# Kernel tuning notes

Measured on AMD Instinct MI355X. Metric: run time of the kernel, lower is better.

## Reference

```python
import jax, jax.numpy as jnp
import numpy as np

N = 50000      # nodes
E = 800000     # edges per metapath
M = 3          # metapaths
H = 2          # heads
IN = 128       # in_dim
HID = 64       # hidden
HEAD = HID // H
OUT = 16       # classes
ATT = 128      # atten_dim


def setup_inputs() -> dict:
    key = jax.random.key(0)
    ks = jax.random.split(key, 12)
    s = 0.05
    return {
        "x": jax.random.normal(ks[0], (N, IN), jnp.float32),
        "edge_index": jax.random.randint(ks[1], (M, 2, E), 0, N, dtype=jnp.int64),
        # per-(metapath, head) GCN params
        "W_enc": jax.random.normal(ks[2], (M, H, IN, HID), jnp.float32) * s,
        "b_enc": jnp.zeros((M, H, HID), jnp.float32),
        "W_conv": jax.random.normal(ks[3], (M, H, HID, HID), jnp.float32) * s,
        "b_conv": jnp.zeros((M, H, HID), jnp.float32),
        "W_dec": jax.random.normal(ks[4], (M, H, HID, HEAD), jnp.float32) * s,
        "b_dec": jnp.zeros((M, H, HEAD), jnp.float32),
        # semantic attention params
        "W_s": jax.random.normal(ks[5], (HID, ATT), jnp.float32) * s,
        "b_s": jnp.zeros((ATT,), jnp.float32),
        "q": jax.random.normal(ks[6], (ATT,), jnp.float32) * s,
        # output projection
        "W_o": jax.random.normal(ks[7], (HID, OUT), jnp.float32) * s,
        "b_o": jnp.zeros((OUT,), jnp.float32),
    }


def _lrelu(v, slope=0.1):
    return jnp.where(v > 0, v, slope * v)


def reference(x, edge_index, W_enc, b_enc, W_conv, b_conv, W_dec, b_dec, W_s, b_s, q, W_o, b_o):
    # encoder for all (metapath, head) at once: [M,H,N,HID]
    h = _lrelu(jnp.einsum('ni,mhio->mhno', x, W_enc) + b_enc[:, :, None, :])

    z_list = []
    for m in range(M):  # small fixed number of metapaths
        src = edge_index[m, 0]
        dst = edge_index[m, 1]
        # GCNConv with self-loops + symmetric normalization (PyG semantics)
        deg = jax.ops.segment_sum(jnp.ones(E, jnp.float32), dst, num_segments=N) + 1.0
        inv_sqrt = jax.lax.rsqrt(deg)
        coef = inv_sqrt[src] * inv_sqrt[dst]                 # [E]
        xw = jnp.einsum('hnd,hdo->hno', h[m], W_conv[m])     # [H,N,HID]
        msg = xw[:, src, :] * coef[None, :, None]            # [H,E,HID] gather
        agg = jax.vmap(lambda mm: jax.ops.segment_sum(mm, dst, num_segments=N))(msg)
        agg = agg + xw * (1.0 / deg)[None, :, None]          # self-loop term (norm = 1/deg)
        agg = agg + b_conv[m][:, None, :]
        hh = _lrelu(agg)
        dec = jnp.einsum('hnd,hdo->hno', hh, W_dec[m]) + b_dec[m][:, None, :]  # [H,N,HEAD]
        z_list.append(jnp.transpose(dec, (1, 0, 2)).reshape(N, HID))           # head concat

    zs = jnp.stack(z_list)                                   # [M,N,HID]
    # semantic attention over metapaths
    hs = jnp.tanh(jnp.einsum('mnd,da->mna', zs, W_s) + b_s)
    beta = jax.nn.softmax(jnp.einsum('mna,a->mn', hs, q).mean(axis=1))  # [M]
    Z = jnp.einsum('m,mnd->nd', beta, zs)                    # [N,HID]
    out = jax.nn.log_softmax(Z @ W_o + b_o, axis=-1)         # [N,OUT]
    return out, beta
```

## Files before the change

### kernel.cpp

```cpp
#include <hip/hip_runtime.h>

#define NN 50000
#define EE 800000
#define MM 3
#define HH 2
#define IND 128
#define HIDD 64
#define HEADD 32
#define OUTD 16
#define ATTD 128

#define NBKT 64
#define BSZ 782

#define NG4 200000
#define BBLK 196
#define QCAP 13200

#define GLS 136

typedef unsigned char u8;
typedef unsigned short u16;
typedef unsigned long long u64;
typedef short bf16x8 __attribute__((ext_vector_type(8)));
typedef unsigned short u16x8 __attribute__((ext_vector_type(8)));
typedef u64 u64x2 __attribute__((ext_vector_type(2)));
typedef float f32x2 __attribute__((ext_vector_type(2)));
typedef float f32x4 __attribute__((ext_vector_type(4)));

__device__ __forceinline__ float lrelu(float v) { return v > 0.f ? v : 0.1f * v; }

__device__ __forceinline__ float fast_tanh(float x) {
    float ax = fabsf(x);
    float e = __expf(-2.0f * ax);
    float t = (1.0f - e) * __builtin_amdgcn_rcpf(1.0f + e);
    return copysignf(t, x);
}

__device__ __forceinline__ u16 f2b(float f) {
    union { float f; unsigned int u; } v; v.f = f;
    unsigned int r = v.u + 0x7fffu + ((v.u >> 16) & 1u);
    return (u16)(r >> 16);
}
__device__ __forceinline__ float b2f(u16 u) {
    union { unsigned int u; float f; } v; v.u = ((unsigned int)u) << 16; return v.f;
}

__device__ __forceinline__ u8 f2e4hw(float f) {
    int r = __builtin_amdgcn_cvt_pk_fp8_f32(f, f, 0, false);
    return (u8)(r & 0xff);
}

__global__ __launch_bounds__(256) void k_bucket(const int* __restrict__ ei,
                                                u64* __restrict__ queues,
                                                int* __restrict__ gcur) {
    __shared__ int cnt[NBKT];
    __shared__ int base[NBKT];
    const int m = blockIdx.y, tid = threadIdx.x;
    const int4* s4 = (const int4*)(ei + (size_t)m * 2 * EE);
    const int4* d4 = (const int4*)(ei + (size_t)m * 2 * EE + EE);
    const int q0 = blockIdx.x * 1024;
    if (tid < NBKT) cnt[tid] = 0;
    __syncthreads();
#pragma unroll
    for (int i = 0; i < 4; i++) {
        int q = q0 + i * 256 + tid;
        if (q < NG4) {
            int4 v = d4[q];
            atomicAdd(&cnt[v.x / BSZ], 1);
            atomicAdd(&cnt[v.y / BSZ], 1);
            atomicAdd(&cnt[v.z / BSZ], 1);
            atomicAdd(&cnt[v.w / BSZ], 1);
        }
    }
    __syncthreads();
    if (tid < NBKT) { base[tid] = atomicAdd(&gcur[m * NBKT + tid], cnt[tid]); cnt[tid] = 0; }
    __syncthreads();
#pragma unroll
    for (int i = 0; i < 4; i++) {
        int q = q0 + i * 256 + tid;
        if (q < NG4) {
            int4 dv = d4[q];
            int4 sv = s4[q];
            int ds[4] = {dv.x, dv.y, dv.z, dv.w};
            int ss[4] = {sv.x, sv.y, sv.z, sv.w};
#pragma unroll
            for (int e = 0; e < 4; e++) {
                int b = ds[e] / BSZ;
                int slot = base[b] + atomicAdd(&cnt[b], 1);
                if (slot < QCAP) {
                    u64 pk = ((u64)(unsigned)ds[e] << 32) | (unsigned)ss[e];
                    queues[((size_t)(m * NBKT + b)) * QCAP + slot] = pk;
                }
            }
        }
    }
}

__global__ void k_pscan(const int* __restrict__ gcur, int* __restrict__ pbase) {
    int t = threadIdx.x;
    if (t < MM) {
        int run = 0;
        for (int b = 0; b < NBKT; b++) {
            int L = gcur[t * NBKT + b]; if (L > QCAP) L = QCAP;
            pbase[t * NBKT + b] = run; run += L;
        }
    }
}

__global__ __launch_bounds__(512) void k_csr(const u64* __restrict__ queues,
                                             const int* __restrict__ gcur,
                                             const int* __restrict__ pbase,
                                             int* __restrict__ ofs,
                                             float* __restrict__ rs,
                                             int* __restrict__ sorted) {
    __shared__ int cnt[BSZ];
    __shared__ int wscan[8];
    const int m = blockIdx.y;
    const int b = blockIdx.x;
    const int tid = threadIdx.x;
    const int lane = tid & 63, w = tid >> 6;
    int qlen = gcur[m * NBKT + b]; if (qlen > QCAP) qlen = QCAP;
    const u64* q = queues + ((size_t)(m * NBKT + b)) * QCAP;
    const u64x2* q2 = (const u64x2*)q;
    const int dlo = b * BSZ;
    const int nd = min(dlo + BSZ, NN) - dlo;
    const int n2 = qlen >> 1;
    for (int i = tid; i < BSZ; i += 512) cnt[i] = 0;
    __syncthreads();
    for (int i = tid; i < n2; i += 512) {
        u64x2 e = q2[i];
        atomicAdd(&cnt[(int)(e.x >> 32) - dlo], 1);
        atomicAdd(&cnt[(int)(e.y >> 32) - dlo], 1);
    }
    if (tid == 0 && (qlen & 1))
        atomicAdd(&cnt[(int)(q[qlen - 1] >> 32) - dlo], 1);
    __syncthreads();
    const int c0 = tid * 2;
    int v0 = (c0 < BSZ) ? cnt[c0] : 0;
    int v1 = (c0 + 1 < BSZ) ? cnt[c0 + 1] : 0;
    int s = v0 + v1;
    int vv = s;
    for (int off = 1; off < 64; off <<= 1) { int t = __shfl_up(vv, off); if (lane >= off) vv += t; }
    if (lane == 63) wscan[w] = vv;
    __syncthreads();
    if (tid == 0) { int run = 0; for (int j = 0; j < 8; j++) { int t = wscan[j]; wscan[j] = run; run += t; } }
    __syncthreads();
    int excl = wscan[w] + vv - s;
    int g0 = pbase[m * NBKT + b] + excl;
    int g1 = g0 + v0;
    if (c0 < nd) {
        ofs[(size_t)m * (NN + 1) + dlo + c0] = g0;
        rs[(size_t)m * NN + dlo + c0] = rsqrtf((float)(v0 + 1));
    }
    if (c0 + 1 < nd) {
        ofs[(size_t)m * (NN + 1) + dlo + c0 + 1] = g1;
        rs[(size_t)m * NN + dlo + c0 + 1] = rsqrtf((float)(v1 + 1));
    }
    if (b == NBKT - 1 && tid == 0)
        ofs[(size_t)m * (NN + 1) + NN] = EE;
    __syncthreads();
    if (c0 < BSZ) cnt[c0] = g0;
    if (c0 + 1 < BSZ) cnt[c0 + 1] = g1;
    __syncthreads();
    int* srt = sorted + (size_t)m * EE;
    for (int i = tid; i < n2; i += 512) {
        u64x2 e = q2[i];
        int p0 = atomicAdd(&cnt[(int)(e.x >> 32) - dlo], 1);
        srt[p0] = (int)(e.x & 0xffffffffu);
        int p1 = atomicAdd(&cnt[(int)(e.y >> 32) - dlo], 1);
        srt[p1] = (int)(e.y & 0xffffffffu);
    }
    if (tid == 0 && (qlen & 1)) {
        u64 e = q[qlen - 1];
        int p0 = atomicAdd(&cnt[(int)(e >> 32) - dlo], 1);
        srt[p0] = (int)(e & 0xffffffffu);
    }
}

__global__ __launch_bounds__(256) void k_prep(const float* __restrict__ We, const float* __restrict__ Wc,
                                              const float* __restrict__ Wd, const float* __restrict__ Ws,
                                              u16* __restrict__ wbe, u16* __restrict__ wbc,
                                              u16* __restrict__ wbd, u16* __restrict__ wbs) {
    int t = blockIdx.x * 256 + threadIdx.x;
    if (t >= 11776) return;
    bf16x8 val;
    u16* dst;
    if (t < 6144) {
        int m = t >> 11, r = t & 2047;
        int nt = r >> 8, ks = (r >> 6) & 3, lane = r & 63;
        int n = nt * 16 + (lane & 15), h = n >> 6, o = n & 63;
        int kb = ks * 32 + (lane >> 4) * 8;
        const float* w = We + ((size_t)(m * 2 + h) * 128) * 64;
#pragma unroll
        for (int j = 0; j < 8; j++) val[j] = (short)f2b(w[(size_t)(kb + j) * 64 + o]);
        dst = wbe + ((size_t)m * 2048 + r) * 8;
    } else if (t < 9216) {
        int u = t - 6144;
        int m = u >> 10, r = u & 1023;
        int nt = r >> 7, ks = (r >> 6) & 1, lane = r & 63;
        int h = nt >> 2, o = (nt & 3) * 16 + (lane & 15);
        int kb = ks * 32 + (lane >> 4) * 8;
        const float* w = Wc + ((size_t)(m * 2 + h) * 64) * 64;
#pragma unroll
        for (int j = 0; j < 8; j++) val[j] = (short)f2b(w[(size_t)(kb + j) * 64 + o]);
        dst = wbc + ((size_t)m * 1024 + r) * 8;
    } else if (t < 10752) {
        int u = t - 9216;
        int m = u >> 9, r = u & 511;
        int nt = r >> 7, ks = (r >> 6) & 1, lane = r & 63;
        int h = nt >> 1, o = (nt & 1) * 16 + (lane & 15);
        int kb = ks * 32 + (lane >> 4) * 8;
        const float* w = Wd + ((size_t)(m * 2 + h) * 64) * 32;
#pragma unroll
        for (int j = 0; j < 8; j++) val[j] = (short)f2b(w[(size_t)(kb + j) * 32 + o]);
        dst = wbd + ((size_t)m * 512 + r) * 8;
    } else {
        int r = t - 10752;
        int nt = r >> 7, ks = (r >> 6) & 1, lane = r & 63;
        int n = nt * 16 + (lane & 15);
        int kb = ks * 32 + (lane >> 4) * 8;
#pragma unroll
        for (int j = 0; j < 8; j++) val[j] = (short)f2b(Ws[(size_t)(kb + j) * 128 + n]);
        dst = wbs + (size_t)r * 8;
    }
    *(bf16x8*)dst = val;
}

#define HLS 133
__global__ __launch_bounds__(256) void k_encconv(const float* __restrict__ x,
                                                 const u16* __restrict__ wbe_all,
                                                 const float* __restrict__ be_all,
                                                 const u16* __restrict__ wbc_all,
                                                 const float* __restrict__ rs_all,
                                                 u8* __restrict__ xw_all) {
    __shared__ float hl[64 * HLS];
    const int m = blockIdx.y;
    const int tid = threadIdx.x, lane = tid & 63, wave = tid >> 6;
    const int quad = lane >> 4, c16 = lane & 15;
    const int row = blockIdx.x * 64 + wave * 16 + c16;
    const bool ok = row < NN;
    const bf16x8* wbE = (const bf16x8*)(wbe_all + (size_t)m * 2048 * 8);
    const float* be = be_all + m * 2 * 64;
    const float* rs = rs_all + (size_t)m * NN;
    u8* xw = xw_all + (size_t)m * NN * 128;
    f32x4 zero = {0.f, 0.f, 0.f, 0.f};
    f32x4 acc[8];
#pragma unroll
    for (int nt = 0; nt < 8; nt++) acc[nt] = zero;
#pragma unroll
    for (int ks = 0; ks < 4; ks++) {
        bf16x8 a = {0, 0, 0, 0, 0, 0, 0, 0};
        if (ok) {
            const float* xp = x + (size_t)row * 128 + ks * 32 + quad * 8;
            float4 xa = *(const float4*)xp;
            float4 xb = *(const float4*)(xp + 4);
            a[0] = (short)f2b(xa.x); a[1] = (short)f2b(xa.y);
            a[2] = (short)f2b(xa.z); a[3] = (short)f2b(xa.w);
            a[4] = (short)f2b(xb.x); a[5] = (short)f2b(xb.y);
            a[6] = (short)f2b(xb.z); a[7] = (short)f2b(xb.w);
        }
#pragma unroll
        for (int nt = 0; nt < 8; nt++)
            acc[nt] = __builtin_amdgcn_mfma_f32_16x16x32_bf16(a, wbE[(nt * 4 + ks) * 64 + lane], acc[nt], 0, 0, 0);
    }
    const int rbl = wave * 16 + quad * 4;
#pragma unroll
    for (int nt = 0; nt < 8; nt++) {
        int col = nt * 16 + c16, hh = col >> 6, o = col & 63;
        float bias = be[hh * 64 + o];
#pragma unroll
        for (int j = 0; j < 4; j++) {
            int rl = rbl + j;
            int rg = blockIdx.x * 64 + rl;
            hl[rl * HLS + col] = (rg < NN) ? lrelu(acc[nt][j] + bias) : 0.f;
        }
    }
    __syncthreads();
    const bf16x8* wbC = (const bf16x8*)(wbc_all + (size_t)m * 1024 * 8);
    f32x4 cacc[8];
#pragma unroll
    for (int nt = 0; nt < 8; nt++) cacc[nt] = zero;
    const int rl = wave * 16 + c16;
#pragma unroll
    for (int ks = 0; ks < 2; ks++) {
        bf16x8 a0, a1;
        const float* hp = &hl[rl * HLS + ks * 32 + quad * 8];
#pragma unroll
        for (int j = 0; j < 8; j++) { a0[j] = (short)f2b(hp[j]); a1[j] = (short)f2b(hp[64 + j]); }
#pragma unroll
        for (int nt = 0; nt < 8; nt++)
            cacc[nt] = __builtin_amdgcn_mfma_f32_16x16x32_bf16(nt < 4 ? a0 : a1, wbC[(nt * 2 + ks) * 64 + lane], cacc[nt], 0, 0, 0);
    }
    float rsv[4];
#pragma unroll
    for (int j = 0; j < 4; j++) {
        int r = blockIdx.x * 64 + rbl + j;
        rsv[j] = (r < NN) ? rs[r] * 64.f : 0.f;
    }
#pragma unroll
    for (int nt = 0; nt < 8; nt++) {
        int col = nt * 16 + c16;
#pragma unroll
        for (int j = 0; j < 4; j++) {
            int r = blockIdx.x * 64 + rbl + j;
            if (r < NN) xw[(size_t)r * 128 + col] = f2e4hw(cacc[nt][j] * rsv[j]);
        }
    }
}

__device__ __forceinline__ void acc_fp8x8(f32x2* acc, u64 w) {
    unsigned lo = (unsigned)w, hi = (unsigned)(w >> 32);
    acc[0] += __builtin_amdgcn_cvt_pk_f32_fp8(lo, false);
    acc[1] += __builtin_amdgcn_cvt_pk_f32_fp8(lo, true);
    acc[2] += __builtin_amdgcn_cvt_pk_f32_fp8(hi, false);
    acc[3] += __builtin_amdgcn_cvt_pk_f32_fp8(hi, true);
}

__global__ __launch_bounds__(512) void k_gpost(const int* __restrict__ sorted_all,
                                               const int* __restrict__ ofs_all,
                                               const float* __restrict__ rs_all,
                                               const u8* __restrict__ xw_all,
                                               const float* __restrict__ bconv_all,
                                               const u16* __restrict__ wbd_all,
                                               const float* __restrict__ bdec_all,
                                               const u16* __restrict__ wbs,
                                               const float* __restrict__ bs,
                                               const float* __restrict__ qv,
                                               u16* __restrict__ z_all,
                                               float* __restrict__ score) {
    __shared__ u16 shm[64 * GLS];
    __shared__ float spart[8];
    u16* ggl = shm;
    float* zl = (float*)shm;
    const int m = blockIdx.y;
    const int tid = threadIdx.x, lane = tid & 63, wave = tid >> 6;
    const int* sorted = sorted_all + (size_t)m * EE;
    const int* ofs = ofs_all + (size_t)m * (NN + 1);
    const float* rs = rs_all + (size_t)m * NN;
    const u8* xw = xw_all + (size_t)m * NN * 128;
    const float* bconv = bconv_all + m * 2 * 64;
    const float* bdec = bdec_all + m * 2 * 32;
    u16* z = z_all + (size_t)m * NN * 64;

    const int p = lane >> 4, c = lane & 15;
    const int base = blockIdx.x * 64 + wave * 8;
    int ov = 0;
    {
        int ii = base + lane;
        if (lane < 9) ov = ofs[ii > NN ? NN : ii];
    }
    auto loadidx = [&](int d) -> int {
        int bg = __shfl(ov, d);
        int dg = __shfl(ov, d + 1) - bg;
        if (base + d >= NN) return 0;
        return (c < dg) ? sorted[bg + c] : 0;
    };
    int idx_cur = loadidx(0);
    for (int d = 0; d < 8; d++) {
        const int dst = base + d;
        const int beg = __shfl(ov, d), end = __shfl(ov, d + 1);
        const int deg = end - beg;
        int idx_nxt = (d < 7) ? loadidx(d + 1) : 0;
        if (dst < NN) {
            u64 ow = *(const u64*)&xw[(size_t)dst * 128 + c * 8];
            f32x2 acc[4];
            acc[0] = 0.f; acc[1] = 0.f; acc[2] = 0.f; acc[3] = 0.f;
            u64 wv[4];
#pragma unroll
            for (int k = 0; k < 4; k++) {
                int e = p + 4 * k;
                int s = __shfl(idx_cur, e);
                wv[k] = (e < deg) ? *(const u64*)&xw[(size_t)s * 128 + c * 8] : 0ull;
            }
#pragma unroll
            for (int k = 0; k < 4; k++) acc_fp8x8(acc, wv[k]);
            int j0 = beg + 16 + p;
            while (j0 < end) {
                int j1 = j0 + 4, j2 = j0 + 8, j3 = j0 + 12;
                bool h1 = j1 < end, h2 = j2 < end, h3 = j3 < end;
                int s0 = sorted[j0];
                int s1 = h1 ? sorted[j1] : s0;
                int s2 = h2 ? sorted[j2] : s0;
                int s3 = h3 ? sorted[j3] : s0;
                u64 w0 = *(const u64*)&xw[(size_t)s0 * 128 + c * 8];
                u64 w1 = h1 ? *(const u64*)&xw[(size_t)s1 * 128 + c * 8] : 0ull;
                u64 w2 = h2 ? *(const u64*)&xw[(size_t)s2 * 128 + c * 8] : 0ull;
                u64 w3 = h3 ? *(const u64*)&xw[(size_t)s3 * 128 + c * 8] : 0ull;
                acc_fp8x8(acc, w0);
                acc_fp8x8(acc, w1);
                acc_fp8x8(acc, w2);
                acc_fp8x8(acc, w3);
                j0 += 16;
            }
#pragma unroll
            for (int k = 0; k < 4; k++) {
                acc[k].x += __shfl_down(acc[k].x, 16);
                acc[k].y += __shfl_down(acc[k].y, 16);
                acc[k].x += __shfl_down(acc[k].x, 32);
                acc[k].y += __shfl_down(acc[k].y, 32);
            }
            if (p == 0) {
                acc_fp8x8(acc, ow);
                float mul = rs[dst] * (1.f / 64.f);
                u16x8 o;
#pragma unroll
                for (int k = 0; k < 4; k++) {
                    o[2 * k] = f2b(acc[k].x * mul);
                    o[2 * k + 1] = f2b(acc[k].y * mul);
                }
                *(u16x8*)&ggl[(wave * 8 + d) * GLS + c * 8] = o;
            }
        } else if (p == 0) {
            u16x8 o = {0, 0, 0, 0, 0, 0, 0, 0};
            *(u16x8*)&ggl[(wave * 8 + d) * GLS + c * 8] = o;
        }
        idx_cur = idx_nxt;
    }
    __syncthreads();

    f32x4 zero = {0.f, 0.f, 0.f, 0.f};
    const int quad = lane >> 4, c16 = lane & 15;
    const int wq = wave & 3, hi = wave >> 2;
    const int rl = wq * 16 + c16;
    const bf16x8* wd = (const bf16x8*)(wbd_all + (size_t)m * 512 * 8);
    f32x4 pacc[2];
    pacc[0] = zero; pacc[1] = zero;
#pragma unroll
    for (int ks = 0; ks < 2; ks++) {
        bf16x8 a;
        int k0 = ks * 32 + quad * 8;
        const u16* gp = &ggl[rl * GLS + hi * 64 + k0];
#pragma unroll
        for (int j = 0; j < 8; j++)
            a[j] = (short)f2b(lrelu(b2f(gp[j]) + bconv[hi * 64 + k0 + j]));
#pragma unroll
        for (int nt2 = 0; nt2 < 2; nt2++) {
            int nt = hi * 2 + nt2;
            pacc[nt2] = __builtin_amdgcn_mfma_f32_16x16x32_bf16(a, wd[(nt * 2 + ks) * 64 + lane], pacc[nt2], 0, 0, 0);
        }
    }
    __syncthreads();
    {
        const int rbl = wq * 16 + quad * 4;
#pragma unroll
        for (int nt2 = 0; nt2 < 2; nt2++) {
            int nt = hi * 2 + nt2;
            int col = nt * 16 + c16, hh = col >> 5, o = col & 31;
            float bias = bdec[hh * 32 + o];
#pragma unroll
            for (int j = 0; j < 4; j++) {
                int rl2 = rbl + j;
                int rg = blockIdx.x * 64 + rl2;
                zl[rl2 * 68 + col] = (rg < NN) ? (pacc[nt2][j] + bias) : 0.f;
            }
        }
    }
    __syncthreads();

    {
        int rl2 = tid >> 3, cq = tid & 7;
        int rg = blockIdx.x * 64 + rl2;
        if (rg < NN) {
#pragma unroll
            for (int i = 0; i < 2; i++) {
                int c4 = (cq * 2 + i) * 4;
                float4 zv = *(const float4*)&zl[rl2 * 68 + c4];
                ushort4 o;
                o.x = f2b(zv.x); o.y = f2b(zv.y); o.z = f2b(zv.z); o.w = f2b(zv.w);
                *(ushort4*)&z[(size_t)rg * 64 + c4] = o;
            }
        }
    }
    float s = 0.f;
    {
        const bf16x8* wsb = (const bf16x8*)wbs;
        f32x4 sa[4];
#pragma unroll
        for (int nt2 = 0; nt2 < 4; nt2++) sa[nt2] = zero;
#pragma unroll
        for (int ks = 0; ks < 2; ks++) {
            bf16x8 a;
            const float* zp = &zl[rl * 68 + ks * 32 + quad * 8];
#pragma unroll
            for (int j = 0; j < 8; j++) a[j] = (short)f2b(zp[j]);
#pragma unroll
            for (int nt2 = 0; nt2 < 4; nt2++) {
                int nt = hi * 4 + nt2;
                sa[nt2] = __builtin_amdgcn_mfma_f32_16x16x32_bf16(a, wsb[(nt * 2 + ks) * 64 + lane], sa[nt2], 0, 0, 0);
            }
        }
        const int rbl = wq * 16 + quad * 4;
#pragma unroll
        for (int nt2 = 0; nt2 < 4; nt2++) {
            int nt = hi * 4 + nt2;
            int col = nt * 16 + c16;
            float qc = qv[col], bb = bs[col];
#pragma unroll
            for (int j = 0; j < 4; j++) {
                int rg = blockIdx.x * 64 + rbl + j;
                if (rg < NN) s += fast_tanh(sa[nt2][j] + bb) * qc;
            }
        }
#pragma unroll
        for (int off = 1; off < 64; off <<= 1) s += __shfl_xor(s, off);
    }
    if (lane == 0) spart[wave] = s;
    __syncthreads();
    if (tid == 0) {
        float t = spart[0] + spart[1] + spart[2] + spart[3]
                + spart[4] + spart[5] + spart[6] + spart[7];
        atomicAdd(&score[m], t);
    }
}

__global__ void k_beta(const float* __restrict__ score, float* __restrict__ beta_ws,
                       float* __restrict__ out) {
    if (threadIdx.x == 0) {
        float s0 = score[0] / (float)NN, s1 = score[1] / (float)NN, s2 = score[2] / (float)NN;
        float mx = fmaxf(s0, fmaxf(s1, s2));
        float e0 = expf(s0 - mx), e1 = expf(s1 - mx), e2 = expf(s2 - mx);
        float inv = 1.f / (e0 + e1 + e2);
        beta_ws[0] = e0 * inv; beta_ws[1] = e1 * inv; beta_ws[2] = e2 * inv;
        out[800000] = e0 * inv; out[800001] = e1 * inv; out[800002] = e2 * inv;
    }
}

__global__ __launch_bounds__(256) void k_out(const u16* __restrict__ z,
                                             const float* __restrict__ beta,
                                             const float* __restrict__ Wo,
                                             const float* __restrict__ bo,
                                             float* __restrict__ out) {
    __shared__ float Zt[64 * 68];
    __shared__ float Wl[64 * 16];
    __shared__ float bl[16];
    const int tid = threadIdx.x, nbase = blockIdx.x * 64;
    float b0 = beta[0], b1 = beta[1], b2 = beta[2];
    for (int qq = tid; qq < 64 * 16; qq += 256) {
        int node = qq >> 4, k4 = qq & 15;
        int ng = nbase + node;
        float4 v = make_float4(0.f, 0.f, 0.f, 0.f);
        if (ng < NN) {
            ushort4 z0 = *(const ushort4*)&z[((size_t)0 * NN + ng) * 64 + k4 * 4];
            ushort4 z1 = *(const ushort4*)&z[((size_t)1 * NN + ng) * 64 + k4 * 4];
            ushort4 z2 = *(const ushort4*)&z[((size_t)2 * NN + ng) * 64 + k4 * 4];
            v.x = b0 * b2f(z0.x) + b1 * b2f(z1.x) + b2 * b2f(z2.x);
            v.y = b0 * b2f(z0.y) + b1 * b2f(z1.y) + b2 * b2f(z2.y);
            v.z = b0 * b2f(z0.z) + b1 * b2f(z1.z) + b2 * b2f(z2.z);
            v.w = b0 * b2f(z0.w) + b1 * b2f(z1.w) + b2 * b2f(z2.w);
        }
        *(float4*)&Zt[node * 68 + k4 * 4] = v;
    }
    for (int qq = tid; qq < 64 * 16 / 4; qq += 256)
        ((float4*)Wl)[qq] = ((const float4*)Wo)[qq];
    if (tid < 16) bl[tid] = bo[tid];
    __syncthreads();

    const int node = tid >> 2, cg = tid & 3;
    float4 a = make_float4(bl[cg * 4 + 0], bl[cg * 4 + 1], bl[cg * 4 + 2], bl[cg * 4 + 3]);
    for (int k = 0; k < 64; k++) {
        float zv = Zt[node * 68 + k];
        float4 w = *(const float4*)&Wl[k * 16 + cg * 4];
        a.x = fmaf(zv, w.x, a.x);
        a.y = fmaf(zv, w.y, a.y);
        a.z = fmaf(zv, w.z, a.z);
        a.w = fmaf(zv, w.w, a.w);
    }
    float mx = fmaxf(fmaxf(a.x, a.y), fmaxf(a.z, a.w));
    mx = fmaxf(mx, __shfl_xor(mx, 1));
    mx = fmaxf(mx, __shfl_xor(mx, 2));
    float sm = expf(a.x - mx) + expf(a.y - mx) + expf(a.z - mx) + expf(a.w - mx);
    sm += __shfl_xor(sm, 1);
    sm += __shfl_xor(sm, 2);
    float lse = mx + logf(sm);
    int ng = nbase + node;
    if (ng < NN) {
        float4 r = make_float4(a.x - lse, a.y - lse, a.z - lse, a.w - lse);
        *(float4*)&out[(size_t)ng * 16 + cg * 4] = r;
    }
}

extern "C" void kernel_launch(void* const* d_in, const int* in_sizes, int n_in,
                              void* d_out, int out_size, void* d_ws, size_t ws_size,
                              hipStream_t stream) {
    const float* x      = (const float*)d_in[0];
    const int*   ei     = (const int*)d_in[1];
    const float* W_enc  = (const float*)d_in[2];
    const float* b_enc  = (const float*)d_in[3];
    const float* W_conv = (const float*)d_in[4];
    const float* b_conv = (const float*)d_in[5];
    const float* W_dec  = (const float*)d_in[6];
    const float* b_dec  = (const float*)d_in[7];
    const float* W_s    = (const float*)d_in[8];
    const float* b_s    = (const float*)d_in[9];
    const float* qv     = (const float*)d_in[10];
    const float* W_o    = (const float*)d_in[11];
    const float* b_o    = (const float*)d_in[12];
    float* out = (float*)d_out;

    char* ws = (char*)d_ws;
    size_t off = 0;
    auto alloc = [&](size_t bytes) -> char* {
        char* p = ws + off;
        off = (off + bytes + 255) & ~(size_t)255;
        return p;
    };
    int*   row_ofs = (int*)alloc((size_t)MM * (NN + 1) * 4);
    float* rs      = (float*)alloc((size_t)MM * NN * 4);
    int*   sorted  = (int*)alloc((size_t)MM * EE * 4);
    u64*   queues  = (u64*)alloc((size_t)MM * NBKT * QCAP * 8);
    int*   gcur    = (int*)alloc((size_t)MM * NBKT * 4);
    int*   pbase   = (int*)alloc((size_t)MM * NBKT * 4);
    float* score   = (float*)alloc(64);
    float* beta_ws = (float*)alloc(64);
    u16*   wbe     = (u16*)alloc((size_t)MM * 2048 * 8 * 2);
    u16*   wbc     = (u16*)alloc((size_t)MM * 1024 * 8 * 2);
    u16*   wbd     = (u16*)alloc((size_t)MM * 512 * 8 * 2);
    u16*   wbs     = (u16*)alloc((size_t)1024 * 8 * 2);
    u8*    xw_buf  = (u8*)alloc((size_t)MM * NN * 128);
    u16*   z_buf   = (u16*)alloc((size_t)MM * NN * 64 * 2);

    hipMemsetAsync(gcur, 0, (size_t)MM * NBKT * 4, stream);
    hipMemsetAsync(score, 0, 16, stream);

    dim3 gbkt(BBLK, MM);
    dim3 gcsr(NBKT, MM);
    k_bucket<<<gbkt, 256, 0, stream>>>(ei, queues, gcur);
    k_pscan<<<1, 64, 0, stream>>>(gcur, pbase);
    k_csr<<<gcsr, 512, 0, stream>>>(queues, gcur, pbase, row_ofs, rs, sorted);
    k_prep<<<46, 256, 0, stream>>>(W_enc, W_conv, W_dec, W_s, wbe, wbc, wbd, wbs);

    const int GB = (NN + 63) / 64;
    dim3 gmm(GB, MM);
    k_encconv<<<gmm, 256, 0, stream>>>(x, wbe, b_enc, wbc, rs, xw_buf);
    k_gpost<<<gmm, 512, 0, stream>>>(sorted, row_ofs, rs, xw_buf,
                                     b_conv, wbd, b_dec, wbs, b_s, qv,
                                     z_buf, score);
    k_beta<<<1, 64, 0, stream>>>(score, beta_ws, out);
    k_out<<<GB, 256, 0, stream>>>(z_buf, beta_ws, W_o, b_o, out);
}
```

Baseline: 276.7 us.

## Gather eight destinations per wave in parallel with double-buffered 16-byte row loads

```diff
diff --git a/kernel.cpp b/kernel.cpp
--- a/kernel.cpp
+++ b/kernel.cpp
@@ -18,6 +18,7 @@
 #define QCAP 13200
 
 #define GLS 136
+#define XWN 50048
 
 typedef unsigned char u8;
 typedef unsigned short u16;
@@ -25,6 +26,7 @@
 typedef short bf16x8 __attribute__((ext_vector_type(8)));
 typedef unsigned short u16x8 __attribute__((ext_vector_type(8)));
 typedef u64 u64x2 __attribute__((ext_vector_type(2)));
+typedef unsigned int u32x4 __attribute__((ext_vector_type(4)));
 typedef float f32x2 __attribute__((ext_vector_type(2)));
 typedef float f32x4 __attribute__((ext_vector_type(4)));
 
@@ -49,6 +51,14 @@
 __device__ __forceinline__ u8 f2e4hw(float f) {
     int r = __builtin_amdgcn_cvt_pk_fp8_f32(f, f, 0, false);
     return (u8)(r & 0xff);
+}
+
+__device__ __forceinline__ void acc16(f32x2* acc, u32x4 w) {
+#pragma unroll
+    for (int i = 0; i < 4; i++) {
+        acc[2 * i]     += __builtin_amdgcn_cvt_pk_f32_fp8(w[i], false);
+        acc[2 * i + 1] += __builtin_amdgcn_cvt_pk_f32_fp8(w[i], true);
+    }
 }
 
 __global__ __launch_bounds__(256) void k_bucket(const int* __restrict__ ei,
@@ -243,7 +253,7 @@
     const bf16x8* wbE = (const bf16x8*)(wbe_all + (size_t)m * 2048 * 8);
     const float* be = be_all + m * 2 * 64;
     const float* rs = rs_all + (size_t)m * NN;
-    u8* xw = xw_all + (size_t)m * NN * 128;
+    u8* xw = xw_all + (size_t)m * XWN * 128;
     f32x4 zero = {0.f, 0.f, 0.f, 0.f};
     f32x4 acc[8];
 #pragma unroll
@@ -304,17 +314,9 @@
 #pragma unroll
         for (int j = 0; j < 4; j++) {
             int r = blockIdx.x * 64 + rbl + j;
-            if (r < NN) xw[(size_t)r * 128 + col] = f2e4hw(cacc[nt][j] * rsv[j]);
-        }
-    }
-}
-
-__device__ __forceinline__ void acc_fp8x8(f32x2* acc, u64 w) {
-    unsigned lo = (unsigned)w, hi = (unsigned)(w >> 32);
-    acc[0] += __builtin_amdgcn_cvt_pk_f32_fp8(lo, false);
-    acc[1] += __builtin_amdgcn_cvt_pk_f32_fp8(lo, true);
-    acc[2] += __builtin_amdgcn_cvt_pk_f32_fp8(hi, false);
-    acc[3] += __builtin_amdgcn_cvt_pk_f32_fp8(hi, true);
+            xw[(size_t)r * 128 + col] = f2e4hw(cacc[nt][j] * rsv[j]);
+        }
+    }
 }
 
 __global__ __launch_bounds__(512) void k_gpost(const int* __restrict__ sorted_all,
@@ -338,84 +340,73 @@
     const int* sorted = sorted_all + (size_t)m * EE;
     const int* ofs = ofs_all + (size_t)m * (NN + 1);
     const float* rs = rs_all + (size_t)m * NN;
-    const u8* xw = xw_all + (size_t)m * NN * 128;
+    const u8* xw = xw_all + (size_t)m * XWN * 128;
     const float* bconv = bconv_all + m * 2 * 64;
     const float* bdec = bdec_all + m * 2 * 32;
     u16* z = z_all + (size_t)m * NN * 64;
 
-    const int p = lane >> 4, c = lane & 15;
-    const int base = blockIdx.x * 64 + wave * 8;
-    int ov = 0;
     {
-        int ii = base + lane;
-        if (lane < 9) ov = ofs[ii > NN ? NN : ii];
-    }
-    auto loadidx = [&](int d) -> int {
-        int bg = __shfl(ov, d);
-        int dg = __shfl(ov, d + 1) - bg;
-        if (base + d >= NN) return 0;
-        return (c < dg) ? sorted[bg + c] : 0;
-    };
-    int idx_cur = loadidx(0);
-    for (int d = 0; d < 8; d++) {
-        const int dst = base + d;
-        const int beg = __shfl(ov, d), end = __shfl(ov, d + 1);
-        const int deg = end - beg;
-        int idx_nxt = (d < 7) ? loadidx(d + 1) : 0;
-        if (dst < NN) {
-            u64 ow = *(const u64*)&xw[(size_t)dst * 128 + c * 8];
-            f32x2 acc[4];
-            acc[0] = 0.f; acc[1] = 0.f; acc[2] = 0.f; acc[3] = 0.f;
-            u64 wv[4];
+        const int g = lane >> 3, c = lane & 7;
+        const int wbase = blockIdx.x * 64 + wave * 8;
+        const int dst = wbase + g;
+        int ov = 0;
+        { int ii = wbase + lane; if (lane < 9) ov = ofs[ii > NN ? NN : ii]; }
+        const int beg = __shfl(ov, g);
+        const int deg = __shfl(ov, g + 1) - beg;
+        int degmax = max(deg, __shfl_xor(deg, 8));
+        degmax = max(degmax, __shfl_xor(degmax, 16));
+        degmax = max(degmax, __shfl_xor(degmax, 32));
+        const int coff = c * 16;
+
+        auto lidx = [&](int j) -> int {
+            int t = j + (c & 3);
+            return (t < deg) ? sorted[beg + t] : NN;
+        };
+        auto lrow = [&](int iv, u32x4* wv) {
 #pragma unroll
             for (int k = 0; k < 4; k++) {
-                int e = p + 4 * k;
-                int s = __shfl(idx_cur, e);
-                wv[k] = (e < deg) ? *(const u64*)&xw[(size_t)s * 128 + c * 8] : 0ull;
+                int s = __shfl(iv, (lane & 0x38) + k);
+                wv[k] = *(const u32x4*)&xw[(size_t)(unsigned)s * 128 + coff];
             }
-#pragma unroll
-            for (int k = 0; k < 4; k++) acc_fp8x8(acc, wv[k]);
-            int j0 = beg + 16 + p;
-            while (j0 < end) {
-                int j1 = j0 + 4, j2 = j0 + 8, j3 = j0 + 12;
-                bool h1 = j1 < end, h2 = j2 < end, h3 = j3 < end;
-                int s0 = sorted[j0];
-                int s1 = h1 ? sorted[j1] : s0;
-                int s2 = h2 ? sorted[j2] : s0;
-                int s3 = h3 ? sorted[j3] : s0;
-                u64 w0 = *(const u64*)&xw[(size_t)s0 * 128 + c * 8];
-                u64 w1 = h1 ? *(const u64*)&xw[(size_t)s1 * 128 + c * 8] : 0ull;
-                u64 w2 = h2 ? *(const u64*)&xw[(size_t)s2 * 128 + c * 8] : 0ull;
-                u64 w3 = h3 ? *(const u64*)&xw[(size_t)s3 * 128 + c * 8] : 0ull;
-                acc_fp8x8(acc, w0);
-                acc_fp8x8(acc, w1);
-                acc_fp8x8(acc, w2);
-                acc_fp8x8(acc, w3);
-                j0 += 16;
-            }
-#pragma unroll
-            for (int k = 0; k < 4; k++) {
-                acc[k].x += __shfl_down(acc[k].x, 16);
-                acc[k].y += __shfl_down(acc[k].y, 16);
-                acc[k].x += __shfl_down(acc[k].x, 32);
-                acc[k].y += __shfl_down(acc[k].y, 32);
-            }
-            if (p == 0) {
-                acc_fp8x8(acc, ow);
-                float mul = rs[dst] * (1.f / 64.f);
-                u16x8 o;
-#pragma unroll
-                for (int k = 0; k < 4; k++) {
-                    o[2 * k] = f2b(acc[k].x * mul);
-                    o[2 * k + 1] = f2b(acc[k].y * mul);
-                }
-                *(u16x8*)&ggl[(wave * 8 + d) * GLS + c * 8] = o;
-            }
-        } else if (p == 0) {
-            u16x8 o = {0, 0, 0, 0, 0, 0, 0, 0};
-            *(u16x8*)&ggl[(wave * 8 + d) * GLS + c * 8] = o;
-        }
-        idx_cur = idx_nxt;
+        };
+
+        f32x2 acc[8];
+#pragma unroll
+        for (int i = 0; i < 8; i++) acc[i] = 0.f;
+
+        int i0 = lidx(0);
+        int i1 = lidx(4);
+        {
+            int sd = dst < NN ? dst : NN;
+            u32x4 w = *(const u32x4*)&xw[(size_t)sd * 128 + coff];
+            acc16(acc, w);
+        }
+        u32x4 wA[4], wB[4];
+        lrow(i0, wA);
+        const int nch = ((degmax + 7) >> 3) * 2;
+        for (int ch = 0; ch < nch; ch += 2) {
+            lrow(i1, wB);
+            i0 = lidx(ch * 4 + 8);
+#pragma unroll
+            for (int k = 0; k < 4; k++) acc16(acc, wA[k]);
+            lrow(i0, wA);
+            i1 = lidx(ch * 4 + 12);
+#pragma unroll
+            for (int k = 0; k < 4; k++) acc16(acc, wB[k]);
+        }
+
+        float rsv = (dst < NN) ? rs[dst] * (1.f / 64.f) : 0.f;
+        u16x8 o0, o1;
+#pragma unroll
+        for (int i = 0; i < 4; i++) {
+            o0[2 * i]     = f2b(acc[i].x * rsv);
+            o0[2 * i + 1] = f2b(acc[i].y * rsv);
+            o1[2 * i]     = f2b(acc[i + 4].x * rsv);
+            o1[2 * i + 1] = f2b(acc[i + 4].y * rsv);
+        }
+        u16* gp = &ggl[(wave * 8 + g) * GLS + coff];
+        *(u16x8*)gp = o0;
+        *(u16x8*)(gp + 8) = o1;
     }
     __syncthreads();
 
@@ -617,7 +608,7 @@
     u16*   wbc     = (u16*)alloc((size_t)MM * 1024 * 8 * 2);
     u16*   wbd     = (u16*)alloc((size_t)MM * 512 * 8 * 2);
     u16*   wbs     = (u16*)alloc((size_t)1024 * 8 * 2);
-    u8*    xw_buf  = (u8*)alloc((size_t)MM * NN * 128);
+    u8*    xw_buf  = (u8*)alloc((size_t)MM * XWN * 128);
     u16*   z_buf   = (u16*)alloc((size_t)MM * NN * 64 * 2);
 
     hipMemsetAsync(gcur, 0, (size_t)MM * NBKT * 4, stream);
```

Result: faster. 248.1 us (-10.3%).
